# Optimization experiments

Hardware: AMD Instinct MI355X
Metric: run time of the kernel (lower is better)

## Reference

```python
import jax, jax.numpy as jnp
import numpy as np

B, S, H, E, I, MAX_K, A_HID = 2, 2048, 1024, 8, 2688, 6, 50


def setup_inputs() -> dict:
    key = jax.random.key(0)
    ks = jax.random.split(key, 10)
    sc = 0.02
    return {
        "hidden_states": jax.random.normal(ks[0], (B, S, H), dtype=jnp.float32),
        "router_w": jax.random.normal(ks[1], (E, H), dtype=jnp.float32) * sc,
        "actor_w1": jax.random.normal(ks[2], (A_HID, H), dtype=jnp.float32) * sc,
        "actor_b1": jnp.zeros((A_HID,), dtype=jnp.float32),
        "actor_w2": jax.random.normal(ks[3], (MAX_K, A_HID), dtype=jnp.float32) * sc,
        "actor_b2": jnp.zeros((MAX_K,), dtype=jnp.float32),
        "gate_w": jax.random.normal(ks[4], (E, I, H), dtype=jnp.float32) * sc,
        "up_w": jax.random.normal(ks[5], (E, I, H), dtype=jnp.float32) * sc,
        "down_w": jax.random.normal(ks[6], (E, H, I), dtype=jnp.float32) * sc,
    }


def reference(hidden_states, router_w, actor_w1, actor_b1, actor_w2, actor_b2,
              gate_w, up_w, down_w):
    # Router: frozen linear -> softmax probs  [B,S,E]
    probs = jax.nn.softmax(
        jnp.einsum("bsh,eh->bse", hidden_states, router_w).astype(jnp.float32),
        axis=-1)

    # Allocator (ActorCritic.actor): Linear -> GELU -> Linear, clamp(-30,30)
    a_h = jax.nn.gelu(jnp.einsum("bsh,ah->bsa", hidden_states, actor_w1) + actor_b1)
    actor_logits = jnp.clip(
        jnp.einsum("bsa,ka->bsk", a_h, actor_w2) + actor_b2, -30.0, 30.0)
    # deterministic per-token k in [1, MAX_K]
    sampled_k = jnp.argmax(actor_logits, axis=-1) + 1  # [B,S] int

    # dynamic_topk_indices_and_scores: iterative argmax+scatter == select the
    # k highest-prob experts per token; keep their scores, zero elsewhere.
    order = jnp.argsort(-probs, axis=-1)           # descending order of experts
    rank = jnp.argsort(order, axis=-1)             # rank[e] = position of expert e
    mask = rank < sampled_k[..., None]             # [B,S,E] bool, top-k selected
    scores = jnp.where(mask, probs, 0.0).astype(hidden_states.dtype)

    # Expert dispatch-combine: out = sum_e scores[...,e] * LlamaMLP_e(x)
    out = jnp.zeros_like(hidden_states)
    for e in range(E):  # fixed small loop over experts
        g = jnp.einsum("bsh,ih->bsi", hidden_states, gate_w[e])
        u = jnp.einsum("bsh,ih->bsi", hidden_states, up_w[e])
        y = jnp.einsum("bsi,hi->bsh", jax.nn.silu(g) * u, down_w[e])
        out = out + scores[..., e:e + 1] * y
    return out
```

## Files before the change

### kernel.cpp

```cpp
#include <hip/hip_runtime.h>
#include <hip/hip_bf16.h>
#include <stdint.h>

#define TOK 4096
#define HD  1024
#define NE  8
#define ID  2688
#define MAXK 6
#define AHID 50
#define NROW 58
#define KCH 64
#define NCH (HD / KCH)

#define BM 128
#define BN 128
#define BK 64
#define NTM (TOK / BM)
#define NID2 (2 * ID)
#define NTN_GUC (NID2 / BN)
#define NB_GUC (NTN_GUC * NTM)
#define NTN_D (HD / BN)
#define NB_D (NTN_D * NTM)
#define CVTB 384

typedef float  f32x4  __attribute__((ext_vector_type(4)));
typedef __bf16 bf16x8 __attribute__((ext_vector_type(8)));
typedef ushort ushort8v __attribute__((ext_vector_type(8)));

__device__ __forceinline__ ushort f2bf(float f) {
  union { float f; uint32_t u; } v; v.f = f;
  return (ushort)((v.u + 0x7FFFu + ((v.u >> 16) & 1u)) >> 16);
}
__device__ __forceinline__ float bf2f(ushort u) {
  union { uint32_t u; float f; } v; v.u = (uint32_t)u << 16; return v.f;
}

#define GLD_LDS16(gp, lp)                                                      \
  __builtin_amdgcn_global_load_lds(                                            \
      (const __attribute__((address_space(1))) uint32_t*)(uintptr_t)(gp),      \
      (__attribute__((address_space(3))) uint32_t*)(uint32_t)(uintptr_t)(lp),  \
      16, 0, 0)

__global__ void k_cvt(const float* __restrict__ src, ushort* __restrict__ dst, int n) {
  int idx = blockIdx.x * blockDim.x + threadIdx.x;
  int stride = gridDim.x * blockDim.x;
  for (int i = idx * 8; i < n; i += stride * 8) {
    float4 a = *(const float4*)(src + i);
    float4 b = *(const float4*)(src + i + 4);
    ushort8v o;
    o[0] = f2bf(a.x); o[1] = f2bf(a.y); o[2] = f2bf(a.z); o[3] = f2bf(a.w);
    o[4] = f2bf(b.x); o[5] = f2bf(b.y); o[6] = f2bf(b.z); o[7] = f2bf(b.w);
    *(ushort8v*)(dst + i) = o;
  }
}

__global__ void k_cvt_gu(const float* __restrict__ g, const float* __restrict__ u,
                         ushort* __restrict__ dst) {
  const int total = NE * NID2 * (HD / 8);
  int idx = blockIdx.x * blockDim.x + threadIdx.x;
  int stride = gridDim.x * blockDim.x;
  for (int i8 = idx; i8 < total; i8 += stride) {
    const int col = (i8 & (HD / 8 - 1)) * 8;
    const int row = i8 >> 7;
    const int e = row / NID2;
    const int q = row - e * NID2;
    const int p = q >> 7, r = q & 127;
    const float* src = ((r < 64) ? g + ((size_t)e * ID + p * 64 + r) * HD
                                 : u + ((size_t)e * ID + p * 64 + (r - 64)) * HD) + col;
    float4 a = *(const float4*)(src);
    float4 b = *(const float4*)(src + 4);
    ushort8v o;
    o[0] = f2bf(a.x); o[1] = f2bf(a.y); o[2] = f2bf(a.z); o[3] = f2bf(a.w);
    o[4] = f2bf(b.x); o[5] = f2bf(b.y); o[6] = f2bf(b.z); o[7] = f2bf(b.w);
    *(ushort8v*)(dst + (size_t)row * HD + col) = o;
  }
}

__global__ __launch_bounds__(256) void k_logits(
    const float* __restrict__ x, const float* __restrict__ rw,
    const float* __restrict__ aw1, float* __restrict__ partial,
    ushort* __restrict__ Xb) {
  __shared__ float xs[256][KCH + 1];
  const int tid = threadIdx.x;
  const int t0 = blockIdx.x * 256;
  const int c = blockIdx.y;
  const int k0 = c * KCH;
#pragma unroll
  for (int j = 0; j < 16; ++j) {
    const int id4 = j * 256 + tid;
    const int row = id4 >> 4;
    const int c4 = (id4 & 15) * 4;
    float4 v = *(const float4*)(x + (size_t)(t0 + row) * HD + k0 + c4);
    xs[row][c4 + 0] = v.x; xs[row][c4 + 1] = v.y;
    xs[row][c4 + 2] = v.z; xs[row][c4 + 3] = v.w;
    ushort4 o; o.x = f2bf(v.x); o.y = f2bf(v.y); o.z = f2bf(v.z); o.w = f2bf(v.w);
    *(ushort4*)(Xb + (size_t)(t0 + row) * HD + k0 + c4) = o;
  }
  __syncthreads();
  float acc[NROW];
#pragma unroll
  for (int r = 0; r < NROW; ++r) acc[r] = 0.f;
  for (int k4 = 0; k4 < KCH; k4 += 4) {
    const float x0 = xs[tid][k4 + 0], x1 = xs[tid][k4 + 1];
    const float x2 = xs[tid][k4 + 2], x3 = xs[tid][k4 + 3];
#pragma unroll
    for (int r = 0; r < NROW; ++r) {
      const float* wp = ((r < NE) ? (rw + (size_t)r * HD)
                                  : (aw1 + (size_t)(r - NE) * HD)) + k0 + k4;
      acc[r] += x0 * wp[0] + x1 * wp[1] + x2 * wp[2] + x3 * wp[3];
    }
  }
  const int t = t0 + tid;
#pragma unroll
  for (int r = 0; r < NROW; ++r)
    partial[((size_t)c * NROW + r) * TOK + t] = acc[r];
}

__global__ __launch_bounds__(256) void k_reduce(
    const float* __restrict__ partial, float* __restrict__ dots) {
  const int t = blockIdx.x * 256 + threadIdx.x;
  const int r = blockIdx.y;
  float s = 0.f;
#pragma unroll
  for (int c = 0; c < NCH; ++c)
    s += partial[((size_t)c * NROW + r) * TOK + t];
  dots[(size_t)r * TOK + t] = s;
}

__global__ __launch_bounds__(64) void k_select(
    const float* __restrict__ dots, const float* __restrict__ ab1_,
    const float* __restrict__ aw2_, const float* __restrict__ ab2_,
    float* __restrict__ scores, int* __restrict__ idx, int* __restrict__ cnt) {
  const int lane = threadIdx.x;
  const int t = blockIdx.x * 64 + lane;
  float d[NROW];
#pragma unroll
  for (int r = 0; r < NROW; ++r) d[r] = dots[(size_t)r * TOK + t];
  float m = d[0];
#pragma unroll
  for (int e = 1; e < NE; ++e) m = fmaxf(m, d[e]);
  float p[NE]; float sum = 0.f;
#pragma unroll
  for (int e = 0; e < NE; ++e) { p[e] = expf(d[e] - m); sum += p[e]; }
  float inv = 1.f / sum;
#pragma unroll
  for (int e = 0; e < NE; ++e) p[e] *= inv;
  float lg[MAXK];
#pragma unroll
  for (int k = 0; k < MAXK; ++k) lg[k] = ab2_[k];
#pragma unroll
  for (int i = 0; i < AHID; ++i) {
    float v = d[NE + i] + ab1_[i];
    float g = 0.5f * v * (1.f + tanhf(0.7978845608028654f * (v + 0.044715f * v * v * v)));
#pragma unroll
    for (int k = 0; k < MAXK; ++k) lg[k] += g * aw2_[k * AHID + i];
  }
  int best = 0; float bv = fminf(fmaxf(lg[0], -30.f), 30.f);
#pragma unroll
  for (int k = 1; k < MAXK; ++k) {
    float lv = fminf(fmaxf(lg[k], -30.f), 30.f);
    if (lv > bv) { bv = lv; best = k; }
  }
  const int kk = best + 1;
  float sc[NE];
#pragma unroll
  for (int e = 0; e < NE; ++e) {
    int rank = 0;
#pragma unroll
    for (int j = 0; j < NE; ++j)
      rank += (p[j] > p[e]) || (p[j] == p[e] && j < e);
    sc[e] = (rank < kk) ? p[e] : 0.f;
    scores[(size_t)t * NE + e] = sc[e];
  }
#pragma unroll
  for (int e = 0; e < NE; ++e) {
    unsigned long long msk = __ballot(sc[e] > 0.f);
    int npop = __popcll(msk);
    int mypos = __popcll(msk & ((1ull << lane) - 1ull));
    int base = 0;
    if (lane == 0 && npop) base = atomicAdd(cnt + e, npop);
    base = __shfl(base, 0);
    if (sc[e] > 0.f) idx[e * TOK + base + mypos] = t;
  }
}

__global__ __launch_bounds__(256, 2) void k_gateupC(
    const ushort* __restrict__ X, const int* __restrict__ idx,
    const int* __restrict__ cnt, const ushort* __restrict__ Wc,
    ushort* __restrict__ act, const int e0, const int actStrideRows,
    const float* __restrict__ dwsrc, ushort* __restrict__ dwdst) {
  __shared__ __attribute__((aligned(16))) ushort lds[BM * BK + BN * BK];
  ushort* As = lds;
  ushort* Bs = lds + BM * BK;

  const int bid = blockIdx.x;
  if (bid >= NB_GUC) {
    if (blockIdx.z != 0) return;
    const int cb = bid - NB_GUC;
    const int ncvt = NE * HD * ID;
    const int stride = CVTB * 256 * 8;
    for (int i = (cb * 256 + threadIdx.x) * 8; i < ncvt; i += stride) {
      float4 a = *(const float4*)(dwsrc + i);
      float4 b = *(const float4*)(dwsrc + i + 4);
      ushort8v o;
      o[0] = f2bf(a.x); o[1] = f2bf(a.y); o[2] = f2bf(a.z); o[3] = f2bf(a.w);
      o[4] = f2bf(b.x); o[5] = f2bf(b.y); o[6] = f2bf(b.z); o[7] = f2bf(b.w);
      *(ushort8v*)(dwdst + i) = o;
    }
    return;
  }

  const int e = e0 + blockIdx.z;
  const int n = cnt[e];
  const int logical = (bid & 7) * (NB_GUC / 8) + (bid >> 3);
  const int tn = logical >> 5;
  const int tm = logical & (NTM - 1);
  const int row0 = tm * BM;
  if (row0 >= n) return;
  const int* idx_e = idx + e * TOK;
  const ushort* WcE = Wc + (size_t)e * NID2 * HD;
  ushort* actE = act + (size_t)actStrideRows * e * ID;

  const int tid = threadIdx.x;
  const int lane = tid & 63;
  const int w = tid >> 6;
  const int wr = (w >> 1) * 64;
  const int wc = (w & 1) * 64;
  const int srow = lane >> 3;
  const int scol = ((lane & 7) ^ srow) * 8;
  const int col0 = tn * BN;

  f32x4 acc[4][4] = {};

  const ushort* pa[4]; const ushort* pb[4];
  ushort* la[4]; ushort* lb[4];
#pragma unroll
  for (int j = 0; j < 4; ++j) {
    const int cc = w * 4 + j;
    const int r = cc * 8 + srow;
    const int token = idx_e[min(row0 + r, n - 1)];
    pa[j] = X   + (size_t)token * HD + scol;
    pb[j] = WcE + (size_t)(col0 + r) * HD + scol;
    la[j] = &As[cc * 512]; lb[j] = &Bs[cc * 512];
  }

  for (int kt = 0; kt < HD / BK; ++kt) {
    const int k0 = kt * BK;
    __syncthreads();
#pragma unroll
    for (int j = 0; j < 4; ++j) {
      GLD_LDS16(pa[j] + k0, la[j]);
      GLD_LDS16(pb[j] + k0, lb[j]);
    }
    __syncthreads();
#pragma unroll
    for (int kk = 0; kk < 2; ++kk) {
      const int kc = kk * 32 + (lane >> 4) * 8;
      const int rr = lane & 15;
      const int kcs = (((kc >> 3) ^ (rr & 7)) << 3);
      bf16x8 af[4], bf_[4];
#pragma unroll
      for (int m = 0; m < 4; ++m)
        af[m] = *(const bf16x8*)&As[(wr + m * 16 + rr) * BK + kcs];
#pragma unroll
      for (int nn = 0; nn < 4; ++nn)
        bf_[nn] = *(const bf16x8*)&Bs[(wc + nn * 16 + rr) * BK + kcs];
#pragma unroll
      for (int m = 0; m < 4; ++m)
#pragma unroll
        for (int nn = 0; nn < 4; ++nn)
          acc[m][nn] = __builtin_amdgcn_mfma_f32_16x16x32_bf16(af[m], bf_[nn], acc[m][nn], 0, 0, 0);
    }
  }

  const int erow = (lane >> 4) * 4, ecol = lane & 15;
  float* exch = (float*)lds;
  __syncthreads();
  if (w & 1) {
#pragma unroll
    for (int m = 0; m < 4; ++m) {
      const int rbase = wr + m * 16 + erow;
#pragma unroll
      for (int nn = 0; nn < 4; ++nn) {
        const int c = nn * 16 + ecol;
#pragma unroll
        for (int j = 0; j < 4; ++j)
          exch[(rbase + j) * 64 + c] = acc[m][nn][j];
      }
    }
  }
  __syncthreads();
  if (!(w & 1)) {
#pragma unroll
    for (int m = 0; m < 4; ++m) {
      const int rbase = wr + m * 16 + erow;
#pragma unroll
      for (int nn = 0; nn < 4; ++nn) {
        const int c = nn * 16 + ecol;
        const int gc = tn * 64 + c;
#pragma unroll
        for (int j = 0; j < 4; ++j) {
          float g = acc[m][nn][j];
          float u = exch[(rbase + j) * 64 + c];
          float h = (g / (1.f + __expf(-g))) * u;
          actE[(size_t)(row0 + rbase + j) * ID + gc] = f2bf(h);
        }
      }
    }
  }
}

__global__ __launch_bounds__(256, 2) void k_down(
    const ushort* __restrict__ act, const ushort* __restrict__ Wd,
    const int* __restrict__ idx, const int* __restrict__ cnt,
    ushort* __restrict__ y) {
  __shared__ __attribute__((aligned(16))) ushort As[BM * BK];
  __shared__ __attribute__((aligned(16))) ushort Bs[BN * BK];

  const int e = blockIdx.z;
  const int n = cnt[e];
  const int bid = blockIdx.x;
  const int logical = (bid & 7) * (NB_D / 8) + (bid >> 3);
  const int tn = logical >> 5;
  const int tm = logical & (NTM - 1);
  const int row0 = tm * BM;
  if (row0 >= n) return;
  const int* idx_e = idx + e * TOK;
  const ushort* A = act + (size_t)e * TOK * ID;
  const ushort* W = Wd + (size_t)e * HD * ID;
  ushort* yE = y + (size_t)e * TOK * HD;

  const int tid = threadIdx.x;
  const int lane = tid & 63;
  const int w = tid >> 6;
  const int wr = (w >> 1) * 64;
  const int wc = (w & 1) * 64;
  const int srow = lane >> 3;
  const int scol = ((lane & 7) ^ srow) * 8;
  const int col0 = tn * BN;

  f32x4 acc[4][4] = {};

  const ushort* pa[4]; const ushort* pb[4];
  ushort* la[4]; ushort* lb[4];
#pragma unroll
  for (int j = 0; j < 4; ++j) {
    const int cc = w * 4 + j;
    const int r = cc * 8 + srow;
    pa[j] = A + (size_t)min(row0 + r, n - 1) * ID + scol;
    pb[j] = W + (size_t)(col0 + r) * ID + scol;
    la[j] = &As[cc * 512]; lb[j] = &Bs[cc * 512];
  }

  for (int kt = 0; kt < ID / BK; ++kt) {
    const int k0 = kt * BK;
    __syncthreads();
#pragma unroll
    for (int j = 0; j < 4; ++j) {
      GLD_LDS16(pa[j] + k0, la[j]);
      GLD_LDS16(pb[j] + k0, lb[j]);
    }
    __syncthreads();
#pragma unroll
    for (int kk = 0; kk < 2; ++kk) {
      const int kc = kk * 32 + (lane >> 4) * 8;
      const int rr = lane & 15;
      const int kcs = (((kc >> 3) ^ (rr & 7)) << 3);
      bf16x8 af[4], bf_[4];
#pragma unroll
      for (int m = 0; m < 4; ++m)
        af[m] = *(const bf16x8*)&As[(wr + m * 16 + rr) * BK + kcs];
#pragma unroll
      for (int nn = 0; nn < 4; ++nn)
        bf_[nn] = *(const bf16x8*)&Bs[(wc + nn * 16 + rr) * BK + kcs];
#pragma unroll
      for (int m = 0; m < 4; ++m)
#pragma unroll
        for (int nn = 0; nn < 4; ++nn)
          acc[m][nn] = __builtin_amdgcn_mfma_f32_16x16x32_bf16(af[m], bf_[nn], acc[m][nn], 0, 0, 0);
    }
  }

  const int erow = (lane >> 4) * 4, ecol = lane & 15;
#pragma unroll
  for (int m = 0; m < 4; ++m) {
    const int cr0 = row0 + wr + m * 16 + erow;
#pragma unroll
    for (int j = 0; j < 4; ++j) {
      const int cr = cr0 + j;
      if (cr < n) {
        const int token = idx_e[cr];
        ushort* yp = yE + (size_t)token * HD + col0 + wc;
#pragma unroll
        for (int nn = 0; nn < 4; ++nn)
          yp[nn * 16 + ecol] = f2bf(acc[m][nn][j]);
      }
    }
  }
}

__global__ __launch_bounds__(256) void k_combine(
    const ushort* __restrict__ y, const float* __restrict__ scores,
    float* __restrict__ out) {
  const int w = threadIdx.x >> 6, lane = threadIdx.x & 63;
  const int t = blockIdx.x * 4 + w;
  const int c0 = lane * 16;
  float acc[16];
#pragma unroll
  for (int i = 0; i < 16; ++i) acc[i] = 0.f;
  const float* sc = scores + (size_t)t * NE;
#pragma unroll
  for (int e = 0; e < NE; ++e) {
    const float s = sc[e];
    if (s > 0.f) {
      const ushort8v* yp = (const ushort8v*)(y + ((size_t)e * TOK + t) * HD + c0);
      ushort8v v0 = yp[0], v1 = yp[1];
#pragma unroll
      for (int i = 0; i < 8; ++i) acc[i] += s * bf2f(v0[i]);
#pragma unroll
      for (int i = 0; i < 8; ++i) acc[8 + i] += s * bf2f(v1[i]);
    }
  }
  float* op = out + (size_t)t * HD + c0;
#pragma unroll
  for (int i = 0; i < 4; ++i)
    *(float4*)(op + 4 * i) = make_float4(acc[4*i], acc[4*i+1], acc[4*i+2], acc[4*i+3]);
}

__global__ __launch_bounds__(256) void k_down64(
    const ushort* __restrict__ act, const ushort* __restrict__ Wd,
    const float* __restrict__ scores, const int* __restrict__ idx,
    const int* __restrict__ cnt, const int e, float* __restrict__ out) {
  __shared__ __attribute__((aligned(16))) ushort As[64 * 64];
  __shared__ __attribute__((aligned(16))) ushort Bs[64 * 64];
  const int n = cnt[e];
  const int row0 = blockIdx.y * 64;
  if (row0 >= n) return;
  const int* idx_e = idx + e * TOK;
  const ushort* A = act;
  const ushort* W = Wd + (size_t)e * HD * ID;
  const int col0 = blockIdx.x * 64;
  const int tid = threadIdx.x, lane = tid & 63, w = tid >> 6;
  const int wr = (w >> 1) * 32, wc = (w & 1) * 32;
  const int srow = lane >> 3, scol = (lane & 7) * 8;
  f32x4 acc[2][2] = {};
  const ushort* pa[2]; const ushort* pb[2];
  ushort* la[2]; ushort* lb[2];
#pragma unroll
  for (int j = 0; j < 2; ++j) {
    const int cc = w * 2 + j;
    const int r = cc * 8 + srow;
    pa[j] = A + (size_t)min(row0 + r, n - 1) * ID + scol;
    pb[j] = W + (size_t)(col0 + r) * ID + scol;
    la[j] = &As[cc * 512]; lb[j] = &Bs[cc * 512];
  }
  for (int kt = 0; kt < ID / 64; ++kt) {
    const int k0 = kt * 64;
    __syncthreads();
#pragma unroll
    for (int j = 0; j < 2; ++j) { GLD_LDS16(pa[j] + k0, la[j]); GLD_LDS16(pb[j] + k0, lb[j]); }
    __syncthreads();
#pragma unroll
    for (int kk = 0; kk < 2; ++kk) {
      const int kc = kk * 32 + (lane >> 4) * 8;
      const int rr = lane & 15;
      bf16x8 af[2], bf_[2];
#pragma unroll
      for (int m = 0; m < 2; ++m) af[m] = *(const bf16x8*)&As[(wr + m * 16 + rr) * 64 + kc];
#pragma unroll
      for (int nn = 0; nn < 2; ++nn) bf_[nn] = *(const bf16x8*)&Bs[(wc + nn * 16 + rr) * 64 + kc];
#pragma unroll
      for (int m = 0; m < 2; ++m)
#pragma unroll
        for (int nn = 0; nn < 2; ++nn)
          acc[m][nn] = __builtin_amdgcn_mfma_f32_16x16x32_bf16(af[m], bf_[nn], acc[m][nn], 0, 0, 0);
    }
  }
  const int erow = (lane >> 4) * 4, ecol = lane & 15;
#pragma unroll
  for (int m = 0; m < 2; ++m) {
    const int cr0 = row0 + wr + m * 16 + erow;
#pragma unroll
    for (int j = 0; j < 4; ++j) {
      const int cr = cr0 + j;
      if (cr < n) {
        const int token = idx_e[cr];
        const float s = scores[(size_t)token * NE + e];
        float* op = out + (size_t)token * HD + col0 + wc;
#pragma unroll
        for (int nn = 0; nn < 2; ++nn) op[nn * 16 + ecol] += s * acc[m][nn][j];
      }
    }
  }
}

extern "C" void kernel_launch(void* const* d_in, const int* in_sizes, int n_in,
                              void* d_out, int out_size, void* d_ws, size_t ws_size,
                              hipStream_t stream) {
  const float* hs       = (const float*)d_in[0];
  const float* router_w = (const float*)d_in[1];
  const float* actor_w1 = (const float*)d_in[2];
  const float* actor_b1 = (const float*)d_in[3];
  const float* actor_w2 = (const float*)d_in[4];
  const float* actor_b2 = (const float*)d_in[5];
  const float* gate_w   = (const float*)d_in[6];
  const float* up_w     = (const float*)d_in[7];
  const float* down_w   = (const float*)d_in[8];
  float* out = (float*)d_out;

  const size_t sz_x    = (size_t)TOK * HD * 2;
  const size_t sz_w    = (size_t)NE * ID * HD * 2;
  const size_t sz_wgu  = 2 * sz_w;
  const size_t sz_act1 = (size_t)TOK * ID * 2;
  const size_t sz_actC = (size_t)NE * TOK * ID * 2;
  const size_t sz_part = (size_t)NCH * NROW * TOK * 4;
  const size_t sz_dt   = (size_t)NROW * TOK * 4;
  const size_t sz_sc   = (size_t)TOK * NE * 4;
  const size_t sz_ix   = (size_t)NE * TOK * 4;

  const size_t fixed = sz_x + sz_wgu + sz_w;
  const size_t tail  = sz_dt + sz_sc + sz_ix + 256;
  const size_t fb_act = (sz_act1 > sz_part ? sz_act1 : sz_part);
  const size_t need_fb = fixed + fb_act + tail;
  const size_t need_cb = fixed + sz_actC + tail;
  if (ws_size < need_fb) return;
  const bool combined = (ws_size >= need_cb);
  const size_t act_sz = combined ? sz_actC : fb_act;

  char* ws = (char*)d_ws;
  ushort* Xb  = (ushort*)ws;
  ushort* Wgu = (ushort*)(ws + sz_x);
  ushort* Wdb = (ushort*)(ws + sz_x + sz_wgu);
  ushort* yb  = Wgu;
  ushort* act = (ushort*)(ws + fixed);
  float*  partial = (float*)(ws + fixed);
  float*  dots   = (float*)(ws + fixed + act_sz);
  float*  scores = (float*)(ws + fixed + act_sz + sz_dt);
  int*    idx    = (int*)  (ws + fixed + act_sz + sz_dt + sz_sc);
  int*    cnt    = (int*)  (ws + fixed + act_sz + sz_dt + sz_sc + sz_ix);

  hipMemsetAsync(cnt, 0, NE * 4, stream);

  k_cvt_gu<<<2048, 256, 0, stream>>>(gate_w, up_w, Wgu);

  k_logits<<<dim3(TOK / 256, NCH), 256, 0, stream>>>(hs, router_w, actor_w1, partial, Xb);
  k_reduce<<<dim3(TOK / 256, NROW), 256, 0, stream>>>(partial, dots);
  k_select<<<TOK / 64, 64, 0, stream>>>(dots, actor_b1, actor_w2, actor_b2,
                                        scores, idx, cnt);

  if (combined) {
    k_gateupC<<<dim3(NB_GUC + CVTB, 1, NE), 256, 0, stream>>>(
        Xb, idx, cnt, Wgu, act, 0, TOK, down_w, Wdb);
    k_down<<<dim3(NB_D, 1, NE), 256, 0, stream>>>(act, Wdb, idx, cnt, yb);
    k_combine<<<TOK / 4, 256, 0, stream>>>(yb, scores, out);
  } else {
    hipMemsetAsync(out, 0, (size_t)TOK * HD * 4, stream);
    k_cvt<<<2048, 256, 0, stream>>>(down_w, Wdb, NE * ID * HD);
    for (int e = 0; e < NE; ++e) {
      k_gateupC<<<dim3(NB_GUC, 1, 1), 256, 0, stream>>>(
          Xb, idx, cnt, Wgu, act, e, 0, nullptr, nullptr);
      k_down64<<<dim3(HD / 64, TOK / 64), 256, 0, stream>>>(
          act, Wdb, scores, idx, cnt, e, out);
    }
  }
}
```

Measured before the change: 480.9 us.

## Fuse gate/up weight conversion into logits kernel, merge reduce into select, persistent down GEMM

Merges the gate/up weight bf16 conversion into the logits launch as extra blocks, so the conversion runs alongside the router/actor dot products. The separate partial-sum reduce kernel is removed and its reduction is done inside the select kernel. The down-projection GEMM becomes a persistent kernel with 768 blocks looping over expert tiles. This cuts launch count and gives better overlap and load balance, at the cost of select reading 16 partial sums per row and a fixed grid for the persistent loop.

```diff
diff --git a/kernel.cpp b/kernel.cpp
--- a/kernel.cpp
+++ b/kernel.cpp
@@ -19,9 +19,10 @@
 #define NID2 (2 * ID)
 #define NTN_GUC (NID2 / BN)
 #define NB_GUC (NTN_GUC * NTM)
-#define NTN_D (HD / BN)
-#define NB_D (NTN_D * NTM)
 #define CVTB 384
+#define NB_D 256
+#define PD_BLOCKS 768
+#define CVTGU 1024
 
 typedef float  f32x4  __attribute__((ext_vector_type(4)));
 typedef __bf16 bf16x8 __attribute__((ext_vector_type(8)));
@@ -54,36 +55,38 @@
   }
 }
 
-__global__ void k_cvt_gu(const float* __restrict__ g, const float* __restrict__ u,
-                         ushort* __restrict__ dst) {
-  const int total = NE * NID2 * (HD / 8);
-  int idx = blockIdx.x * blockDim.x + threadIdx.x;
-  int stride = gridDim.x * blockDim.x;
-  for (int i8 = idx; i8 < total; i8 += stride) {
-    const int col = (i8 & (HD / 8 - 1)) * 8;
-    const int row = i8 >> 7;
-    const int e = row / NID2;
-    const int q = row - e * NID2;
-    const int p = q >> 7, r = q & 127;
-    const float* src = ((r < 64) ? g + ((size_t)e * ID + p * 64 + r) * HD
-                                 : u + ((size_t)e * ID + p * 64 + (r - 64)) * HD) + col;
-    float4 a = *(const float4*)(src);
-    float4 b = *(const float4*)(src + 4);
-    ushort8v o;
-    o[0] = f2bf(a.x); o[1] = f2bf(a.y); o[2] = f2bf(a.z); o[3] = f2bf(a.w);
-    o[4] = f2bf(b.x); o[5] = f2bf(b.y); o[6] = f2bf(b.z); o[7] = f2bf(b.w);
-    *(ushort8v*)(dst + (size_t)row * HD + col) = o;
-  }
-}
-
-__global__ __launch_bounds__(256) void k_logits(
+__global__ __launch_bounds__(256) void k_logitsF(
     const float* __restrict__ x, const float* __restrict__ rw,
     const float* __restrict__ aw1, float* __restrict__ partial,
-    ushort* __restrict__ Xb) {
+    ushort* __restrict__ Xb,
+    const float* __restrict__ g, const float* __restrict__ u,
+    ushort* __restrict__ Wgu) {
+  const int bid = blockIdx.x;
+  const int tid = threadIdx.x;
+  if (bid >= 256) {
+    const int cb = bid - 256;
+    const int total = NE * NID2 * (HD / 8);
+    const int stride = CVTGU * 256;
+    for (int i8 = cb * 256 + tid; i8 < total; i8 += stride) {
+      const int col = (i8 & (HD / 8 - 1)) * 8;
+      const int row = i8 >> 7;
+      const int e = row / NID2;
+      const int q = row - e * NID2;
+      const int p = q >> 7, r = q & 127;
+      const float* src = ((r < 64) ? g + ((size_t)e * ID + p * 64 + r) * HD
+                                   : u + ((size_t)e * ID + p * 64 + (r - 64)) * HD) + col;
+      float4 a = *(const float4*)(src);
+      float4 b = *(const float4*)(src + 4);
+      ushort8v o;
+      o[0] = f2bf(a.x); o[1] = f2bf(a.y); o[2] = f2bf(a.z); o[3] = f2bf(a.w);
+      o[4] = f2bf(b.x); o[5] = f2bf(b.y); o[6] = f2bf(b.z); o[7] = f2bf(b.w);
+      *(ushort8v*)(Wgu + (size_t)row * HD + col) = o;
+    }
+    return;
+  }
   __shared__ float xs[256][KCH + 1];
-  const int tid = threadIdx.x;
-  const int t0 = blockIdx.x * 256;
-  const int c = blockIdx.y;
+  const int c = bid >> 4;
+  const int t0 = (bid & 15) * 256;
   const int k0 = c * KCH;
 #pragma unroll
   for (int j = 0; j < 16; ++j) {
@@ -116,26 +119,21 @@
     partial[((size_t)c * NROW + r) * TOK + t] = acc[r];
 }
 
-__global__ __launch_bounds__(256) void k_reduce(
-    const float* __restrict__ partial, float* __restrict__ dots) {
-  const int t = blockIdx.x * 256 + threadIdx.x;
-  const int r = blockIdx.y;
-  float s = 0.f;
-#pragma unroll
-  for (int c = 0; c < NCH; ++c)
-    s += partial[((size_t)c * NROW + r) * TOK + t];
-  dots[(size_t)r * TOK + t] = s;
-}
-
-__global__ __launch_bounds__(64) void k_select(
-    const float* __restrict__ dots, const float* __restrict__ ab1_,
+__global__ __launch_bounds__(64) void k_select2(
+    const float* __restrict__ partial, const float* __restrict__ ab1_,
     const float* __restrict__ aw2_, const float* __restrict__ ab2_,
     float* __restrict__ scores, int* __restrict__ idx, int* __restrict__ cnt) {
   const int lane = threadIdx.x;
   const int t = blockIdx.x * 64 + lane;
   float d[NROW];
 #pragma unroll
-  for (int r = 0; r < NROW; ++r) d[r] = dots[(size_t)r * TOK + t];
+  for (int r = 0; r < NROW; ++r) {
+    float s = 0.f;
+#pragma unroll
+    for (int c = 0; c < NCH; ++c)
+      s += partial[((size_t)c * NROW + r) * TOK + t];
+    d[r] = s;
+  }
   float m = d[0];
 #pragma unroll
   for (int e = 1; e < NE; ++e) m = fmaxf(m, d[e]);
@@ -151,9 +149,9 @@
 #pragma unroll
   for (int i = 0; i < AHID; ++i) {
     float v = d[NE + i] + ab1_[i];
-    float g = 0.5f * v * (1.f + tanhf(0.7978845608028654f * (v + 0.044715f * v * v * v)));
-#pragma unroll
-    for (int k = 0; k < MAXK; ++k) lg[k] += g * aw2_[k * AHID + i];
+    float gg = 0.5f * v * (1.f + tanhf(0.7978845608028654f * (v + 0.044715f * v * v * v)));
+#pragma unroll
+    for (int k = 0; k < MAXK; ++k) lg[k] += gg * aw2_[k * AHID + i];
   }
   int best = 0; float bv = fminf(fmaxf(lg[0], -30.f), 30.f);
 #pragma unroll
@@ -199,7 +197,7 @@
     const int cb = bid - NB_GUC;
     const int ncvt = NE * HD * ID;
     const int stride = CVTB * 256 * 8;
-    for (int i = (cb * 256 + threadIdx.x) * 8; i < ncvt; i += stride) {
+    for (int i = (cb * 256 + (int)threadIdx.x) * 8; i < ncvt; i += stride) {
       float4 a = *(const float4*)(dwsrc + i);
       float4 b = *(const float4*)(dwsrc + i + 4);
       ushort8v o;
@@ -310,25 +308,12 @@
   }
 }
 
-__global__ __launch_bounds__(256, 2) void k_down(
+__global__ __launch_bounds__(256, 2) void k_downP(
     const ushort* __restrict__ act, const ushort* __restrict__ Wd,
     const int* __restrict__ idx, const int* __restrict__ cnt,
     ushort* __restrict__ y) {
   __shared__ __attribute__((aligned(16))) ushort As[BM * BK];
   __shared__ __attribute__((aligned(16))) ushort Bs[BN * BK];
-
-  const int e = blockIdx.z;
-  const int n = cnt[e];
-  const int bid = blockIdx.x;
-  const int logical = (bid & 7) * (NB_D / 8) + (bid >> 3);
-  const int tn = logical >> 5;
-  const int tm = logical & (NTM - 1);
-  const int row0 = tm * BM;
-  if (row0 >= n) return;
-  const int* idx_e = idx + e * TOK;
-  const ushort* A = act + (size_t)e * TOK * ID;
-  const ushort* W = Wd + (size_t)e * HD * ID;
-  ushort* yE = y + (size_t)e * TOK * HD;
 
   const int tid = threadIdx.x;
   const int lane = tid & 63;
@@ -337,63 +322,78 @@
   const int wc = (w & 1) * 64;
   const int srow = lane >> 3;
   const int scol = ((lane & 7) ^ srow) * 8;
-  const int col0 = tn * BN;
-
-  f32x4 acc[4][4] = {};
-
-  const ushort* pa[4]; const ushort* pb[4];
-  ushort* la[4]; ushort* lb[4];
-#pragma unroll
-  for (int j = 0; j < 4; ++j) {
-    const int cc = w * 4 + j;
-    const int r = cc * 8 + srow;
-    pa[j] = A + (size_t)min(row0 + r, n - 1) * ID + scol;
-    pb[j] = W + (size_t)(col0 + r) * ID + scol;
-    la[j] = &As[cc * 512]; lb[j] = &Bs[cc * 512];
-  }
-
-  for (int kt = 0; kt < ID / BK; ++kt) {
-    const int k0 = kt * BK;
-    __syncthreads();
+  const int erow = (lane >> 4) * 4, ecol = lane & 15;
+
+  for (int item = blockIdx.x; item < NE * NB_D; item += PD_BLOCKS) {
+    const int e = item >> 8;
+    const int bid = item & (NB_D - 1);
+    const int logical = (bid & 7) * (NB_D / 8) + (bid >> 3);
+    const int tn = logical >> 5;
+    const int tm = logical & (NTM - 1);
+    const int n = cnt[e];
+    const int row0 = tm * BM;
+    if (row0 >= n) continue;
+    const int* idx_e = idx + e * TOK;
+    const ushort* A = act + (size_t)e * TOK * ID;
+    const ushort* W = Wd + (size_t)e * HD * ID;
+    ushort* yE = y + (size_t)e * TOK * HD;
+    const int col0 = tn * BN;
+
+    f32x4 acc[4][4] = {};
+
+    const ushort* pa[4]; const ushort* pb[4];
+    ushort* la[4]; ushort* lb[4];
 #pragma unroll
     for (int j = 0; j < 4; ++j) {
-      GLD_LDS16(pa[j] + k0, la[j]);
-      GLD_LDS16(pb[j] + k0, lb[j]);
-    }
-    __syncthreads();
-#pragma unroll
-    for (int kk = 0; kk < 2; ++kk) {
-      const int kc = kk * 32 + (lane >> 4) * 8;
-      const int rr = lane & 15;
-      const int kcs = (((kc >> 3) ^ (rr & 7)) << 3);
-      bf16x8 af[4], bf_[4];
-#pragma unroll
-      for (int m = 0; m < 4; ++m)
-        af[m] = *(const bf16x8*)&As[(wr + m * 16 + rr) * BK + kcs];
-#pragma unroll
-      for (int nn = 0; nn < 4; ++nn)
-        bf_[nn] = *(const bf16x8*)&Bs[(wc + nn * 16 + rr) * BK + kcs];
-#pragma unroll
-      for (int m = 0; m < 4; ++m)
+      const int cc = w * 4 + j;
+      const int r = cc * 8 + srow;
+      pa[j] = A + (size_t)min(row0 + r, n - 1) * ID + scol;
+      pb[j] = W + (size_t)(col0 + r) * ID + scol;
+      la[j] = &As[cc * 512]; lb[j] = &Bs[cc * 512];
+    }
+
+    for (int kt = 0; kt < ID / BK; ++kt) {
+      const int k0 = kt * BK;
+      __syncthreads();
+#pragma unroll
+      for (int j = 0; j < 4; ++j) {
+        GLD_LDS16(pa[j] + k0, la[j]);
+        GLD_LDS16(pb[j] + k0, lb[j]);
+      }
+      __syncthreads();
+#pragma unroll
+      for (int kk = 0; kk < 2; ++kk) {
+        const int kc = kk * 32 + (lane >> 4) * 8;
+        const int rr = lane & 15;
+        const int kcs = (((kc >> 3) ^ (rr & 7)) << 3);
+        bf16x8 af[4], bf_[4];
+#pragma unroll
+        for (int m = 0; m < 4; ++m)
+          af[m] = *(const bf16x8*)&As[(wr + m * 16 + rr) * BK + kcs];
 #pragma unroll
         for (int nn = 0; nn < 4; ++nn)
-          acc[m][nn] = __builtin_amdgcn_mfma_f32_16x16x32_bf16(af[m], bf_[nn], acc[m][nn], 0, 0, 0);
-    }
-  }
-
-  const int erow = (lane >> 4) * 4, ecol = lane & 15;
-#pragma unroll
-  for (int m = 0; m < 4; ++m) {
-    const int cr0 = row0 + wr + m * 16 + erow;
-#pragma unroll
-    for (int j = 0; j < 4; ++j) {
-      const int cr = cr0 + j;
-      if (cr < n) {
-        const int token = idx_e[cr];
-        ushort* yp = yE + (size_t)token * HD + col0 + wc;
-#pragma unroll
-        for (int nn = 0; nn < 4; ++nn)
-          yp[nn * 16 + ecol] = f2bf(acc[m][nn][j]);
+          bf_[nn] = *(const bf16x8*)&Bs[(wc + nn * 16 + rr) * BK + kcs];
+#pragma unroll
+        for (int m = 0; m < 4; ++m)
+#pragma unroll
+          for (int nn = 0; nn < 4; ++nn)
+            acc[m][nn] = __builtin_amdgcn_mfma_f32_16x16x32_bf16(af[m], bf_[nn], acc[m][nn], 0, 0, 0);
+      }
+    }
+
+#pragma unroll
+    for (int m = 0; m < 4; ++m) {
+      const int cr0 = row0 + wr + m * 16 + erow;
+#pragma unroll
+      for (int j = 0; j < 4; ++j) {
+        const int cr = cr0 + j;
+        if (cr < n) {
+          const int token = idx_e[cr];
+          ushort* yp = yE + (size_t)token * HD + col0 + wc;
+#pragma unroll
+          for (int nn = 0; nn < 4; ++nn)
+            yp[nn * 16 + ecol] = f2bf(acc[m][nn][j]);
+        }
       }
     }
   }
@@ -534,24 +534,21 @@
   ushort* yb  = Wgu;
   ushort* act = (ushort*)(ws + fixed);
   float*  partial = (float*)(ws + fixed);
-  float*  dots   = (float*)(ws + fixed + act_sz);
   float*  scores = (float*)(ws + fixed + act_sz + sz_dt);
   int*    idx    = (int*)  (ws + fixed + act_sz + sz_dt + sz_sc);
   int*    cnt    = (int*)  (ws + fixed + act_sz + sz_dt + sz_sc + sz_ix);
 
   hipMemsetAsync(cnt, 0, NE * 4, stream);
 
-  k_cvt_gu<<<2048, 256, 0, stream>>>(gate_w, up_w, Wgu);
-
-  k_logits<<<dim3(TOK / 256, NCH), 256, 0, stream>>>(hs, router_w, actor_w1, partial, Xb);
-  k_reduce<<<dim3(TOK / 256, NROW), 256, 0, stream>>>(partial, dots);
-  k_select<<<TOK / 64, 64, 0, stream>>>(dots, actor_b1, actor_w2, actor_b2,
-                                        scores, idx, cnt);
+  k_logitsF<<<256 + CVTGU, 256, 0, stream>>>(hs, router_w, actor_w1, partial, Xb,
+                                             gate_w, up_w, Wgu);
+  k_select2<<<TOK / 64, 64, 0, stream>>>(partial, actor_b1, actor_w2, actor_b2,
+                                         scores, idx, cnt);
 
   if (combined) {
     k_gateupC<<<dim3(NB_GUC + CVTB, 1, NE), 256, 0, stream>>>(
         Xb, idx, cnt, Wgu, act, 0, TOK, down_w, Wdb);
-    k_down<<<dim3(NB_D, 1, NE), 256, 0, stream>>>(act, Wdb, idx, cnt, yb);
+    k_downP<<<PD_BLOCKS, 256, 0, stream>>>(act, Wdb, idx, cnt, yb);
     k_combine<<<TOK / 4, 256, 0, stream>>>(yb, scores, out);
   } else {
     hipMemsetAsync(out, 0, (size_t)TOK * HD * 4, stream);
```

New measurement: 718.7 us. 49.5% more time.
